# Kernel tuning notes

Measured on AMD Instinct MI355X. Metric: run time of the kernel, lower is better.

## Reference

```python
import jax, jax.numpy as jnp
import numpy as np

B, S, D, E = 8, 4096, 4096, 64
CAP_FACTOR = 1.1


def setup_inputs() -> dict:
    key = jax.random.key(0)
    k1, k2 = jax.random.split(key)
    x = jax.random.normal(k1, (B, S, D), jnp.float32)
    # original zero-inits the router weight (degenerate routing); use small random
    # weights so top-2 routing is non-trivial. Forward math is identical.
    W = jax.random.normal(k2, (E, D), jnp.float32) * 0.02
    return {"x": x, "W": W}


def reference(x, W):
    b, s, d = x.shape
    e = W.shape[0]
    tokens = b * s
    capacity = int(tokens * CAP_FACTOR * 2 / e)  # static Python int

    # router: logits = x @ W^T (nn.Linear, no bias)
    logits = jnp.einsum('bsd,ed->bse', x, W)
    probs = jax.nn.softmax(logits, axis=-1)

    top2_p, top2_i = jax.lax.top_k(probs, 2)            # [b,s,2]
    top2_pn = top2_p / top2_p.sum(-1, keepdims=True)     # renormalized top-2 probs

    # Flatten the (token, slot) pairs in the same (i,j,k) enumeration order as
    # the reference triple loop; stable argsort reproduces its tie-breaking.
    n2 = tokens * 2
    e_flat = top2_i.reshape(n2)                          # expert id per slot
    p_flat = top2_pn.reshape(n2)                         # prob per slot
    onehot = e_flat[:, None] == jnp.arange(e)[None, :]   # [n2, e] bool

    # per-expert rank of each assigned slot by descending prob (stable)
    pe = jnp.where(onehot, p_flat[:, None], -jnp.inf)    # [n2, e]
    order = jnp.argsort(-pe, axis=0)                     # stable sort, desc prob
    rank = jnp.argsort(order, axis=0)                    # rank of slot within expert
    keep = onehot & (rank < capacity)                    # capacity truncation

    keep = keep.reshape(b, s, 2, e)
    dispatch = keep.any(axis=2).astype(x.dtype)                       # [b,s,e]
    combine = (keep.astype(x.dtype) * top2_pn[..., None]).sum(axis=2)  # [b,s,e]

    # aux loss: uses pre-truncation counts (expert_counts in the loop counts all
    # top-2 assignments, before capacity dropping)
    prob_per_expert = probs.sum(axis=(0, 1)) / tokens
    counts = onehot.sum(axis=0).astype(x.dtype)
    usage = counts / counts.sum()
    aux_loss = (prob_per_expert * usage).sum() * e

    return dispatch, combine, probs, aux_loss
```

## Files before the change

kernel.cpp:

```cpp
#include <hip/hip_runtime.h>
#include <hip/hip_bf16.h>
#include <cstdint>
#include <cstddef>

#define TOKENS   32768
#define DDIM     4096
#define NEXP     64
#define N2       65536
#define CAPACITY 1126
#define KSPLIT   2
#define KHALF    (DDIM / KSPLIT)
#define BK       32
#define TT       128

#define WS_PART  0
#define WS_PFLAT (16u << 20)
#define WS_EFLAT ((16u << 20) + 262144u)
#define WS_PSUM  ((16u << 20) + 524288u)
#define WS_CNT   ((16u << 20) + 524288u + 256u)

__global__ void zero_kernel(float* __restrict__ dc, float* __restrict__ psum) {
    int idx = blockIdx.x * blockDim.x + threadIdx.x;
    float4 z = make_float4(0.f, 0.f, 0.f, 0.f);
    const int n4 = (2 * TOKENS * NEXP) / 4;
    for (int i = idx; i < n4; i += gridDim.x * blockDim.x)
        ((float4*)dc)[i] = z;
    if (idx < NEXP) psum[idx] = 0.f;
}

__launch_bounds__(128, 1)
__global__ void gemm_logits(const float* __restrict__ x, const float* __restrict__ W,
                            float* __restrict__ part) {
    __shared__ __align__(16) float xs[2][TT * BK];
    __shared__ __align__(16) float wt[2][NEXP * BK];

    const int tid  = threadIdx.x;
    const int lane = tid & 63;
    const int wv   = tid >> 6;
    const int tx   = tid & 7;
    const int ty   = tid >> 3;
    const int kh   = blockIdx.x & 1;
    const int tok0 = (blockIdx.x >> 1) * TT;
    const int d0b  = kh * KHALF;

    const int srow = lane >> 3;
    const int scol = lane & 7;

    auto stage = [&](int p, int c) {
#pragma unroll
        for (int qq = 0; qq < 8; ++qq) {
            int q = wv * 8 + qq;
            int r = q * 8 + srow;
            const float* g = x + (size_t)(tok0 + r) * DDIM + d0b + c * BK
                               + 4 * (scol ^ (q & 7));
            __builtin_amdgcn_global_load_lds(
                (const __attribute__((address_space(1))) void*)g,
                (__attribute__((address_space(3))) void*)&xs[p][q * 8 * BK],
                16, 0, 0);
        }
#pragma unroll
        for (int qq = 0; qq < 4; ++qq) {
            int q = wv * 4 + qq;
            int e = q * 8 + srow;
            const float* g = W + (size_t)e * DDIM + d0b + c * BK
                               + 4 * (scol ^ (q & 7));
            __builtin_amdgcn_global_load_lds(
                (const __attribute__((address_space(1))) void*)g,
                (__attribute__((address_space(3))) void*)&wt[p][q * 8 * BK],
                16, 0, 0);
        }
    };

    float tot[8][8];
#pragma unroll
    for (int i = 0; i < 8; ++i)
#pragma unroll
        for (int j = 0; j < 8; ++j) tot[i][j] = 0.f;

    stage(0, 0);

    const int NCHUNK = KHALF / BK;
    for (int c = 0; c < NCHUNK; ++c) {
        const int p = c & 1;
        __syncthreads();
        if (c + 1 < NCHUNK) stage(p ^ 1, c + 1);

#pragma unroll
        for (int g = 0; g < 8; ++g) {
            float4 xr[8], wr[8];
#pragma unroll
            for (int i = 0; i < 8; ++i)
                xr[i] = *(const float4*)&xs[p][(ty * 8 + i) * BK + 4 * (g ^ (ty & 7))];
#pragma unroll
            for (int j = 0; j < 8; ++j)
                wr[j] = *(const float4*)&wt[p][(tx * 8 + j) * BK + 4 * (g ^ (tx & 7))];
#pragma unroll
            for (int i = 0; i < 8; ++i)
#pragma unroll
                for (int j = 0; j < 8; ++j) {
                    tot[i][j] = fmaf(xr[i].x, wr[j].x, tot[i][j]);
                    tot[i][j] = fmaf(xr[i].y, wr[j].y, tot[i][j]);
                    tot[i][j] = fmaf(xr[i].z, wr[j].z, tot[i][j]);
                    tot[i][j] = fmaf(xr[i].w, wr[j].w, tot[i][j]);
                }
        }
    }

    float* o = part + ((size_t)kh * TOKENS + tok0) * 64;
#pragma unroll
    for (int i = 0; i < 8; ++i) {
        int row = ty * 8 + i;
        *(float4*)&o[(size_t)row * 64 + tx * 8 + 0] =
            make_float4(tot[i][0], tot[i][1], tot[i][2], tot[i][3]);
        *(float4*)&o[(size_t)row * 64 + tx * 8 + 4] =
            make_float4(tot[i][4], tot[i][5], tot[i][6], tot[i][7]);
    }
}

__launch_bounds__(256, 2)
__global__ void combine_kernel(const float* __restrict__ part,
                               float* __restrict__ probs_out,
                               float* __restrict__ p_flat,
                               int* __restrict__ e_flat,
                               float* __restrict__ psum) {
    __shared__ __align__(16) float L[128][68];
    __shared__ float red[256];
    const int tid  = threadIdx.x;
    const int tok0 = blockIdx.x * 128;
    const size_t base = (size_t)tok0 * 64;

#pragma unroll
    for (int i = 0; i < 8; ++i) {
        int idx4 = i * 256 + tid;
        float4 a0 = ((const float4*)(part + 0ull * TOKENS * 64 + base))[idx4];
        float4 a1 = ((const float4*)(part + 1ull * TOKENS * 64 + base))[idx4];
        float4 s = make_float4(a0.x + a1.x, a0.y + a1.y, a0.z + a1.z, a0.w + a1.w);
        int row = idx4 >> 4, col = (idx4 & 15) * 4;
        *(float4*)&L[row][col] = s;
    }
    __syncthreads();

    if (tid < 128) {
        const int t = tid;
        float m = -INFINITY;
#pragma unroll
        for (int e = 0; e < 64; ++e) m = fmaxf(m, L[t][e]);
        float s = 0.f;
#pragma unroll
        for (int e = 0; e < 64; ++e) {
            float v = expf(L[t][e] - m);
            L[t][e] = v;
            s += v;
        }
        float p1 = -1.f, p2 = -1.f; int i1 = 0, i2 = 0;
#pragma unroll
        for (int e = 0; e < 64; ++e) {
            float p = L[t][e] / s;
            L[t][e] = p;
            if (p > p1)      { p2 = p1; i2 = i1; p1 = p; i1 = e; }
            else if (p > p2) { p2 = p;  i2 = e; }
        }
        float rs = p1 + p2;
        int g = tok0 + t;
        p_flat[2 * g]     = p1 / rs;
        p_flat[2 * g + 1] = p2 / rs;
        e_flat[2 * g]     = i1;
        e_flat[2 * g + 1] = i2;
    }
    __syncthreads();

#pragma unroll
    for (int i = 0; i < 8; ++i) {
        int idx4 = i * 256 + tid;
        int row = idx4 >> 4, col = (idx4 & 15) * 4;
        ((float4*)(probs_out + base))[idx4] = *(const float4*)&L[row][col];
    }

    float acc = 0.f;
    {
        int e = tid & 63, rg = (tid >> 6) * 32;
#pragma unroll
        for (int r = 0; r < 32; ++r) acc += L[rg + r][e];
    }
    red[tid] = acc;
    __syncthreads();
    if (tid < 64) {
        float v = red[tid] + red[tid + 64] + red[tid + 128] + red[tid + 192];
        atomicAdd(&psum[tid], v);
    }
}

__launch_bounds__(256, 2)
__global__ void expert_sort_kernel(const float* __restrict__ p_flat,
                                   const int* __restrict__ e_flat,
                                   float* __restrict__ dispatch,
                                   float* __restrict__ combine,
                                   int* __restrict__ counts) {
    __shared__ unsigned long long keys[4096];
    __shared__ int cnt;
    const int tid = threadIdx.x;
    const int e   = blockIdx.x;

    if (tid == 0) cnt = 0;
    __syncthreads();

    for (int i4 = tid; i4 < N2 / 4; i4 += 256) {
        int4 ev = ((const int4*)e_flat)[i4];
        int slot = i4 * 4;
#pragma unroll
        for (int j = 0; j < 4; ++j) {
            int ee = (j == 0) ? ev.x : (j == 1) ? ev.y : (j == 2) ? ev.z : ev.w;
            if (ee == e) {
                float p = p_flat[slot + j];
                int pos = atomicAdd(&cnt, 1);
                if (pos < 4096)
                    keys[pos] = ((unsigned long long)__float_as_uint(p) << 32) |
                                (unsigned long long)(0xFFFFFFFFu - (unsigned)(slot + j));
            }
        }
    }
    __syncthreads();
    const int n = cnt;

    if (n > CAPACITY) {
        int m = 2048;
        while (m < n) m <<= 1;
        for (int i = tid; i < m; i += 256)
            if (i >= n) keys[i] = 0ull;
        __syncthreads();

        for (int k = 2; k <= m; k <<= 1) {
            for (int j = k >> 1; j > 0; j >>= 1) {
                for (int i = tid; i < m; i += 256) {
                    int ixj = i ^ j;
                    if (ixj > i) {
                        bool desc = ((i & k) == 0);
                        unsigned long long a = keys[i], b = keys[ixj];
                        bool sw = desc ? (a < b) : (a > b);
                        if (sw) { keys[i] = b; keys[ixj] = a; }
                    }
                }
                __syncthreads();
            }
        }
    }

    int lim = n < CAPACITY ? n : CAPACITY;
    for (int pos = tid; pos < lim; pos += 256) {
        unsigned long long key = keys[pos];
        unsigned slot = 0xFFFFFFFFu - (unsigned)(key & 0xFFFFFFFFull);
        float p = __uint_as_float((unsigned)(key >> 32));
        int token = (int)(slot >> 1);
        dispatch[(size_t)token * 64 + e] = 1.0f;
        combine [(size_t)token * 64 + e] = p;
    }
    if (tid == 0) counts[e] = n;
}

__global__ void aux_kernel(const float* __restrict__ psum,
                           const int* __restrict__ counts,
                           float* __restrict__ out_aux) {
    int tid = threadIdx.x;
    float v = (psum[tid] / (float)TOKENS) * ((float)counts[tid] / (float)N2);
    for (int off = 32; off > 0; off >>= 1) v += __shfl_down(v, off, 64);
    if (tid == 0) *out_aux = v * (float)NEXP;
}

extern "C" void kernel_launch(void* const* d_in, const int* in_sizes, int n_in,
                              void* d_out, int out_size, void* d_ws, size_t ws_size,
                              hipStream_t stream) {
    (void)in_sizes; (void)n_in; (void)out_size; (void)ws_size;

    const float* x = (const float*)d_in[0];
    const float* W = (const float*)d_in[1];

    float* out      = (float*)d_out;
    float* dispatch = out;
    float* combine  = out + (size_t)TOKENS * NEXP;
    float* probs    = out + (size_t)2 * TOKENS * NEXP;
    float* aux      = out + (size_t)3 * TOKENS * NEXP;

    char*  ws     = (char*)d_ws;
    float* part   = (float*)(ws + WS_PART);
    float* p_flat = (float*)(ws + WS_PFLAT);
    int*   e_flat = (int*)  (ws + WS_EFLAT);
    float* psum   = (float*)(ws + WS_PSUM);
    int*   counts = (int*)  (ws + WS_CNT);

    zero_kernel<<<1024, 256, 0, stream>>>(dispatch, psum);
    gemm_logits<<<512, 128, 0, stream>>>(x, W, part);
    combine_kernel<<<256, 256, 0, stream>>>(part, probs, p_flat, e_flat, psum);
    expert_sort_kernel<<<64, 256, 0, stream>>>(p_flat, e_flat, dispatch, combine, counts);
    aux_kernel<<<1, 64, 0, stream>>>(psum, counts, aux);
}
```

Before: 985.0 us.

## Restructure router GEMM: one token per lane, W transposed and read uniformly, 4-way K split

The router GEMM moves from a 128x64 LDS-tiled outer product to one token per lane with 64 accumulators. Each wave owns its own quarter of K and streams only x through LDS. A new kernel pre-transposes W into a [D][64] layout so every lane in a wave reads the same W addresses, allowing scalar or broadcast loads. Barriers are replaced by per-wave vmcnt waits, the grid is doubled with a 4-way K split, and the combine kernel now sums four partials, which doubles partial-buffer traffic and adds a transpose launch.

New measurement: 1.124 ms. +14.1%, slower.

```diff
diff --git a/kernel.cpp b/kernel.cpp
--- a/kernel.cpp
+++ b/kernel.cpp
@@ -8,16 +8,16 @@
 #define NEXP     64
 #define N2       65536
 #define CAPACITY 1126
-#define KSPLIT   2
-#define KHALF    (DDIM / KSPLIT)
+#define KSPLIT   4
+#define KQ       (DDIM / KSPLIT)
 #define BK       32
-#define TT       128
 
 #define WS_PART  0
-#define WS_PFLAT (16u << 20)
-#define WS_EFLAT ((16u << 20) + 262144u)
-#define WS_PSUM  ((16u << 20) + 524288u)
-#define WS_CNT   ((16u << 20) + 524288u + 256u)
+#define WS_PFLAT (32u << 20)
+#define WS_EFLAT ((32u << 20) + 262144u)
+#define WS_PSUM  ((32u << 20) + 524288u)
+#define WS_CNT   ((32u << 20) + 524288u + 256u)
+#define WS_WT    (34u << 20)
 
 __global__ void zero_kernel(float* __restrict__ dc, float* __restrict__ psum) {
     int idx = blockIdx.x * blockDim.x + threadIdx.x;
@@ -28,93 +28,100 @@
     if (idx < NEXP) psum[idx] = 0.f;
 }
 
-__launch_bounds__(128, 1)
-__global__ void gemm_logits(const float* __restrict__ x, const float* __restrict__ W,
-                            float* __restrict__ part) {
-    __shared__ __align__(16) float xs[2][TT * BK];
-    __shared__ __align__(16) float wt[2][NEXP * BK];
+__global__ void wtrans_kernel(const float* __restrict__ W, float* __restrict__ Wt) {
+    __shared__ float T[64][65];
+    const int tid = threadIdx.x;
+    const int d0  = blockIdx.x * 64;
+    {
+        int e = tid & 63, ip = tid >> 6;
+#pragma unroll
+        for (int jj = 0; jj < 4; ++jj) {
+            int j = ip * 4 + jj;
+            float4 v = *(const float4*)&W[(size_t)e * DDIM + d0 + j * 4];
+            T[e][j * 4 + 0] = v.x; T[e][j * 4 + 1] = v.y;
+            T[e][j * 4 + 2] = v.z; T[e][j * 4 + 3] = v.w;
+        }
+    }
+    __syncthreads();
+    {
+        int r = tid >> 2, eg = tid & 3;
+#pragma unroll
+        for (int mm = 0; mm < 4; ++mm) {
+            int e0 = eg * 16 + mm * 4;
+            float4 v = make_float4(T[e0][r], T[e0 + 1][r], T[e0 + 2][r], T[e0 + 3][r]);
+            *(float4*)&Wt[(size_t)(d0 + r) * 64 + e0] = v;
+        }
+    }
+}
+
+__global__ __launch_bounds__(128, 2)
+void gemm_logits(const float* __restrict__ x, const float* __restrict__ Wt,
+                 float* __restrict__ part) {
+    __shared__ __align__(16) float xb[2][2][2048];
 
     const int tid  = threadIdx.x;
     const int lane = tid & 63;
     const int wv   = tid >> 6;
-    const int tx   = tid & 7;
-    const int ty   = tid >> 3;
-    const int kh   = blockIdx.x & 1;
-    const int tok0 = (blockIdx.x >> 1) * TT;
-    const int d0b  = kh * KHALF;
-
-    const int srow = lane >> 3;
-    const int scol = lane & 7;
+    const int wvu  = __builtin_amdgcn_readfirstlane(wv);
+    const int qu   = __builtin_amdgcn_readfirstlane((blockIdx.x & 1) * 2 + wv);
+    const int tb   = (blockIdx.x >> 1) * 64;
+    const int t    = tb + lane;
+    const int k0   = qu * KQ;
+
+    const int sr = lane >> 3;
+    const int sc = lane & 7;
 
     auto stage = [&](int p, int c) {
 #pragma unroll
-        for (int qq = 0; qq < 8; ++qq) {
-            int q = wv * 8 + qq;
-            int r = q * 8 + srow;
-            const float* g = x + (size_t)(tok0 + r) * DDIM + d0b + c * BK
-                               + 4 * (scol ^ (q & 7));
+        for (int i = 0; i < 8; ++i) {
+            int r = i * 8 + sr;
+            const float* g = x + (size_t)(tb + r) * DDIM + k0 + c * BK
+                               + 4 * (sc ^ (r & 7));
             __builtin_amdgcn_global_load_lds(
                 (const __attribute__((address_space(1))) void*)g,
-                (__attribute__((address_space(3))) void*)&xs[p][q * 8 * BK],
+                (__attribute__((address_space(3))) void*)&xb[wvu][p][i * 256],
                 16, 0, 0);
         }
-#pragma unroll
-        for (int qq = 0; qq < 4; ++qq) {
-            int q = wv * 4 + qq;
-            int e = q * 8 + srow;
-            const float* g = W + (size_t)e * DDIM + d0b + c * BK
-                               + 4 * (scol ^ (q & 7));
-            __builtin_amdgcn_global_load_lds(
-                (const __attribute__((address_space(1))) void*)g,
-                (__attribute__((address_space(3))) void*)&wt[p][q * 8 * BK],
-                16, 0, 0);
-        }
     };
 
-    float tot[8][8];
-#pragma unroll
-    for (int i = 0; i < 8; ++i)
-#pragma unroll
-        for (int j = 0; j < 8; ++j) tot[i][j] = 0.f;
+    float acc[64];
+#pragma unroll
+    for (int e = 0; e < 64; ++e) acc[e] = 0.f;
 
     stage(0, 0);
 
-    const int NCHUNK = KHALF / BK;
+    const int NCHUNK = KQ / BK;
     for (int c = 0; c < NCHUNK; ++c) {
         const int p = c & 1;
-        __syncthreads();
-        if (c + 1 < NCHUNK) stage(p ^ 1, c + 1);
-
-#pragma unroll
-        for (int g = 0; g < 8; ++g) {
-            float4 xr[8], wr[8];
-#pragma unroll
-            for (int i = 0; i < 8; ++i)
-                xr[i] = *(const float4*)&xs[p][(ty * 8 + i) * BK + 4 * (g ^ (ty & 7))];
-#pragma unroll
-            for (int j = 0; j < 8; ++j)
-                wr[j] = *(const float4*)&wt[p][(tx * 8 + j) * BK + 4 * (g ^ (tx & 7))];
-#pragma unroll
-            for (int i = 0; i < 8; ++i)
-#pragma unroll
-                for (int j = 0; j < 8; ++j) {
-                    tot[i][j] = fmaf(xr[i].x, wr[j].x, tot[i][j]);
-                    tot[i][j] = fmaf(xr[i].y, wr[j].y, tot[i][j]);
-                    tot[i][j] = fmaf(xr[i].z, wr[j].z, tot[i][j]);
-                    tot[i][j] = fmaf(xr[i].w, wr[j].w, tot[i][j]);
-                }
-        }
-    }
-
-    float* o = part + ((size_t)kh * TOKENS + tok0) * 64;
-#pragma unroll
-    for (int i = 0; i < 8; ++i) {
-        int row = ty * 8 + i;
-        *(float4*)&o[(size_t)row * 64 + tx * 8 + 0] =
-            make_float4(tot[i][0], tot[i][1], tot[i][2], tot[i][3]);
-        *(float4*)&o[(size_t)row * 64 + tx * 8 + 4] =
-            make_float4(tot[i][4], tot[i][5], tot[i][6], tot[i][7]);
-    }
+        if (c + 1 < NCHUNK) {
+            stage(p ^ 1, c + 1);
+            asm volatile("s_waitcnt vmcnt(8)" ::: "memory");
+        } else {
+            asm volatile("s_waitcnt vmcnt(0)" ::: "memory");
+        }
+        __builtin_amdgcn_sched_barrier(0);
+
+        const float* __restrict__ wrow = Wt + (size_t)(k0 + c * BK) * 64;
+#pragma unroll 2
+        for (int k4 = 0; k4 < 8; ++k4) {
+            float4 xr = *(const float4*)&xb[wvu][p][lane * 32 + 4 * (k4 ^ (lane & 7))];
+#pragma unroll
+            for (int kk = 0; kk < 4; ++kk) {
+                float xv = (kk == 0) ? xr.x : (kk == 1) ? xr.y : (kk == 2) ? xr.z : xr.w;
+                const float* __restrict__ wr = wrow + (k4 * 4 + kk) * 64;
+#pragma unroll
+                for (int e = 0; e < 64; ++e)
+                    acc[e] = fmaf(xv, wr[e], acc[e]);
+            }
+        }
+    }
+
+    float* o = part + ((size_t)qu * TOKENS + t) * 64;
+#pragma unroll
+    for (int e4 = 0; e4 < 16; ++e4)
+        *(float4*)&o[e4 * 4] =
+            make_float4(acc[e4 * 4 + 0], acc[e4 * 4 + 1],
+                        acc[e4 * 4 + 2], acc[e4 * 4 + 3]);
 }
 
 __launch_bounds__(256, 2)
@@ -134,7 +141,12 @@
         int idx4 = i * 256 + tid;
         float4 a0 = ((const float4*)(part + 0ull * TOKENS * 64 + base))[idx4];
         float4 a1 = ((const float4*)(part + 1ull * TOKENS * 64 + base))[idx4];
-        float4 s = make_float4(a0.x + a1.x, a0.y + a1.y, a0.z + a1.z, a0.w + a1.w);
+        float4 a2 = ((const float4*)(part + 2ull * TOKENS * 64 + base))[idx4];
+        float4 a3 = ((const float4*)(part + 3ull * TOKENS * 64 + base))[idx4];
+        float4 s = make_float4((a0.x + a1.x) + (a2.x + a3.x),
+                               (a0.y + a1.y) + (a2.y + a3.y),
+                               (a0.z + a1.z) + (a2.z + a3.z),
+                               (a0.w + a1.w) + (a2.w + a3.w));
         int row = idx4 >> 4, col = (idx4 & 15) * 4;
         *(float4*)&L[row][col] = s;
     }
@@ -286,9 +298,11 @@
     int*   e_flat = (int*)  (ws + WS_EFLAT);
     float* psum   = (float*)(ws + WS_PSUM);
     int*   counts = (int*)  (ws + WS_CNT);
+    float* Wt     = (float*)(ws + WS_WT);
 
     zero_kernel<<<1024, 256, 0, stream>>>(dispatch, psum);
-    gemm_logits<<<512, 128, 0, stream>>>(x, W, part);
+    wtrans_kernel<<<64, 256, 0, stream>>>(W, Wt);
+    gemm_logits<<<1024, 128, 0, stream>>>(x, Wt, part);
     combine_kernel<<<256, 256, 0, stream>>>(part, probs, p_flat, e_flat, psum);
     expert_sort_kernel<<<64, 256, 0, stream>>>(p_flat, e_flat, dispatch, combine, counts);
     aux_kernel<<<1, 64, 0, stream>>>(psum, counts, aux);
```
